# Kernel optimization log

Hardware: AMD Instinct MI355X
Metric: run time of the kernel (lower is better)

The kernel has to match this reference:

```python
import jax, jax.numpy as jnp
import numpy as np

# Static problem sizes (uniform ragged batch -> dense-packable)
B, NC, NP, C = 16, 128, 256, 128
HID = 2 * C            # mlp_hidden_scale * embedding_channels
COORD_SCALE = 5.0      # args.coord_scale
DIS_THRES = 10.0       # args.dis_map_thres
N_PROT = 16384         # total protein_whole residues
MAXN = 2 + NC + NP     # per-sample complex length (glb_c + compound + glb_p + pocket)


def setup_inputs() -> dict:
    key = jax.random.key(0)
    ks = jax.random.split(key, 12)
    protein_feats = jax.random.normal(ks[0], (N_PROT, 1280), jnp.float32)
    compound_feats = jax.random.normal(ks[1], (B * NC, 56), jnp.float32)
    complex_coords = jax.random.normal(ks[2], (B * MAXN, 3), jnp.float32) * 10.0
    dis_map = jax.random.uniform(ks[3], (B * NP * NC,), jnp.float32) * DIS_THRES
    keep_idx = jnp.sort(jax.random.randint(ks[4], (B * NP,), 0, N_PROT))
    glb_c = jnp.ones((1, C), jnp.float32)
    glb_p = jnp.ones((1, C), jnp.float32)
    # xavier_uniform with gain=0.001 ~ tiny weights
    W_prot = jax.random.normal(ks[5], (1280, C), jnp.float32) * 0.001
    b_prot = jnp.zeros((C,), jnp.float32)
    W_comp = jax.random.normal(ks[6], (56, C), jnp.float32) * 0.001
    b_comp = jnp.zeros((C,), jnp.float32)
    W1 = jax.random.normal(ks[7], (C, HID), jnp.float32) / np.sqrt(C)
    b1 = jnp.zeros((HID,), jnp.float32)
    W2 = jax.random.normal(ks[8], (HID, 1), jnp.float32) / np.sqrt(HID)
    b2 = jnp.zeros((1,), jnp.float32)
    return dict(protein_feats=protein_feats, compound_feats=compound_feats,
                complex_coords=complex_coords, dis_map=dis_map, keep_idx=keep_idx,
                glb_c=glb_c, glb_p=glb_p, W_prot=W_prot, b_prot=b_prot,
                W_comp=W_comp, b_comp=b_comp, W1=W1, b1=b1, W2=W2, b2=b2)


def reference(protein_feats, compound_feats, complex_coords, dis_map, keep_idx,
              glb_c, glb_p, W_prot, b_prot, W_comp, b_comp, W1, b1, W2, b2):
    # --- input projections + keepNode gather (pocket residues from whole protein)
    pocket_emb = (protein_feats[keep_idx] @ W_prot + b_prot).reshape(B, NP, C)
    compound_emb = (compound_feats @ W_comp + b_comp).reshape(B, NC, C)

    # --- ragged batch assembly: per-sample [glb_c, compound_i, glb_p, pocket_i]
    # (uniform sizes -> single dense concat replaces the Python loop of mask+cat)
    gc = jnp.broadcast_to(glb_c[None], (B, 1, C))
    gp = jnp.broadcast_to(glb_p[None], (B, 1, C))
    new_samples = jnp.concatenate([gc, compound_emb, gp, pocket_emb], axis=1)  # [B, MAXN, C]

    # --- stand-in pair embedding for EfficientMCAttModel output:
    # pair_embed_batched[b, i, j] over (glb_p+pocket) x (glb_c+compound)
    p_side = new_samples[:, NC + 1:, :]     # [B, NP+1, C]
    c_side = new_samples[:, :NC + 1, :]     # [B, NC+1, C]
    pair = p_side[:, :, None, :] + c_side[:, None, :, :]  # [B, NP+1, NC+1, C]

    # --- coordinates (normalize, split by segment/is_global layout)
    coords = (complex_coords / COORD_SCALE).reshape(B, MAXN, 3)
    compound_coords_n = coords[:, 1:NC + 1, :]   # [B, NC, 3]
    pocket_coords_n = coords[:, NC + 2:, :]      # [B, NP, 3]

    # --- cdist(pocket, compound)  [B, NP, NC]
    diff = pocket_coords_n[:, :, None, :] - compound_coords_n[:, None, :, :]
    dmap = jnp.sqrt(jnp.sum(diff * diff, axis=-1) + 1e-12)

    # --- distmap MLP on z = pair[:, 1:, 1:] then sigmoid * thres
    z = pair[:, 1:, 1:, :]                        # [B, NP, NC, C]
    h = jax.nn.relu(z @ W1 + b1)                  # [B, NP, NC, HID]
    logits = (h @ W2 + b2)[..., 0]                # [B, NP, NC]
    # z_mask = outer(pocket_mask, compound_mask) is all-True for uniform sizes
    y_pred = jax.nn.sigmoid(logits).reshape(-1) * DIS_THRES
    y_pred_by_coords = jnp.clip(dmap.reshape(-1) * COORD_SCALE, 0.0, DIS_THRES)

    compound_coords_out = compound_coords_n.reshape(-1, 3) * COORD_SCALE
    pocket_coords_out = pocket_coords_n.reshape(-1, 3) * COORD_SCALE
    compound_batch = jnp.repeat(jnp.arange(B, dtype=jnp.int32), NC)
    pocket_batch = jnp.repeat(jnp.arange(B, dtype=jnp.int32), NP)
    keepNode_less_5 = jnp.zeros((), jnp.int32)
    return (compound_coords_out, compound_batch, pocket_coords_out, pocket_batch,
            y_pred, y_pred_by_coords, dis_map, keepNode_less_5)
```

## Files before the change

kernel.cpp:

```cpp
#include <hip/hip_runtime.h>
#include <hip/hip_bf16.h>
#include <cstddef>


typedef __attribute__((ext_vector_type(8))) short short8v;
typedef __attribute__((ext_vector_type(4))) float f32x4;
typedef _Float16 half2v __attribute__((ext_vector_type(2)));
typedef _Float16 half8v __attribute__((ext_vector_type(8)));

__device__ __forceinline__ unsigned int f2bf(float x) {
    unsigned int u = __float_as_uint(x);
    return (u + 0x7fffu + ((u >> 16) & 1u)) >> 16;
}

__device__ __forceinline__ float dot8h(half8v r, half8v w, float acc) {
#if __has_builtin(__builtin_amdgcn_fdot2)
#pragma unroll
    for (int q = 0; q < 4; ++q) {
        half2v rq = {r[2 * q], r[2 * q + 1]};
        half2v wq = {w[2 * q], w[2 * q + 1]};
        acc = __builtin_amdgcn_fdot2(rq, wq, acc, false);
    }
#else
#pragma unroll
    for (int q = 0; q < 8; ++q) acc += (float)r[q] * (float)w[q];
#endif
    return acc;
}

#define WS_WTP   0u
#define WS_WTC   655360u
#define WS_BP1   688128u
#define WS_BC1   689152u
#define WS_W2H   690176u
#define WS_P1H   691200u
#define WS_PPH   3836928u

__global__ __launch_bounds__(256) void k_fusew(const float* __restrict__ Wp,
                                               const float* __restrict__ Wc,
                                               const float* __restrict__ bp,
                                               const float* __restrict__ bc,
                                               const float* __restrict__ W1,
                                               const float* __restrict__ b1,
                                               const float* __restrict__ W2,
                                               const float* __restrict__ coords,
                                               const float* __restrict__ dism,
                                               float* __restrict__ out,
                                               char* __restrict__ ws) {
    const int tid = threadIdx.x, bid = blockIdx.x;

    if (bid >= 168) {
        const int g = (bid - 168) * 256 + tid;
        {
            const float4* src = reinterpret_cast<const float4*>(dism + (size_t)g * 8);
            float4* dst = reinterpret_cast<float4*>(out + 1073152 + (size_t)g * 8);
            dst[0] = src[0]; dst[1] = src[1];
        }
        if (g < 6144) {
            const int row = g / 3, d = g - row * 3;
            const int bb2 = row >> 7, c = row & 127;
            const float x = coords[(size_t)(bb2 * 386 + 1 + c) * 3 + d];
            out[g] = (x / 5.0f) * 5.0f;
        }
        if (g < 2048) out[6144 + g] = (float)(g >> 7);
        if (g < 12288) {
            const int row = g / 3, d = g - row * 3;
            const int bb2 = row >> 8, p = row & 255;
            const float x = coords[(size_t)(bb2 * 386 + 130 + p) * 3 + d];
            out[8192 + g] = (x / 5.0f) * 5.0f;
        }
        if (g < 4096) out[20480 + g] = (float)(g >> 8);
        if (g == 0) out[1597440] = 0.0f;
        return;
    }

    __shared__ float Al[8][128];
    const int row0 = bid * 8;
    {
        const int r = tid >> 5, k4 = (tid & 31) * 4;
        const int rg = row0 + r;
        float4 v = make_float4(0.f, 0.f, 0.f, 0.f);
        if (rg < 1280)       v = *reinterpret_cast<const float4*>(Wp + (size_t)rg * 128 + k4);
        else if (rg < 1336)  v = *reinterpret_cast<const float4*>(Wc + (size_t)(rg - 1280) * 128 + k4);
        else if (rg == 1336) v = *reinterpret_cast<const float4*>(bp + k4);
        else if (rg == 1337) v = *reinterpret_cast<const float4*>(bc + k4);
        *reinterpret_cast<float4*>(&Al[r][k4]) = v;
    }
    __syncthreads();
    float acc[8];
#pragma unroll
    for (int r = 0; r < 8; ++r) acc[r] = 0.f;
#pragma unroll 4
    for (int k4 = 0; k4 < 128; k4 += 4) {
        float w0 = W1[(k4 + 0) * 256 + tid];
        float w1 = W1[(k4 + 1) * 256 + tid];
        float w2 = W1[(k4 + 2) * 256 + tid];
        float w3 = W1[(k4 + 3) * 256 + tid];
#pragma unroll
        for (int r = 0; r < 8; ++r) {
            float4 a = *reinterpret_cast<const float4*>(&Al[r][k4]);
            acc[r] += a.x * w0 + a.y * w1 + a.z * w2 + a.w * w3;
        }
    }
    if (bid < 160) {
        unsigned int w[4];
#pragma unroll
        for (int q = 0; q < 4; ++q)
            w[q] = f2bf(acc[2 * q]) | (f2bf(acc[2 * q + 1]) << 16);
        unsigned short* WtP = (unsigned short*)(ws + WS_WTP);
        *reinterpret_cast<uint4*>(WtP + (size_t)tid * 1280 + row0) = make_uint4(w[0], w[1], w[2], w[3]);
    } else if (bid < 167) {
        unsigned int w[4];
#pragma unroll
        for (int q = 0; q < 4; ++q)
            w[q] = f2bf(acc[2 * q]) | (f2bf(acc[2 * q + 1]) << 16);
        unsigned short* WtC = (unsigned short*)(ws + WS_WTC);
        *reinterpret_cast<uint4*>(WtC + (size_t)tid * 64 + (row0 - 1280)) = make_uint4(w[0], w[1], w[2], w[3]);
    } else {
        ((float*)(ws + WS_BP1))[tid] = acc[0] + b1[tid];
        ((float*)(ws + WS_BC1))[tid] = acc[1];
        ((_Float16*)(ws + WS_W2H))[tid] = (_Float16)W2[tid];
        unsigned short* WtC = (unsigned short*)(ws + WS_WTC);
        *reinterpret_cast<uint4*>(WtC + (size_t)tid * 64 + 56) = make_uint4(0, 0, 0, 0);
    }
}

struct AB { float4 ra[2]; uint4 rb[8]; };

__device__ __forceinline__ void load_tile(AB& t, bool pocket, int koff,
                                          const float* __restrict__ prot,
                                          const float* __restrict__ comp,
                                          const int* keepL, int m0,
                                          const unsigned short* __restrict__ Bt,
                                          int bstride, int tid) {
#pragma unroll
    for (int u = 0; u < 2; ++u) {
        const int unit = tid + 256 * u;
        const int r = unit >> 4, kc = unit & 15;
        float4 v = make_float4(0.f, 0.f, 0.f, 0.f);
        if (pocket) {
            v = *reinterpret_cast<const float4*>(prot + (size_t)keepL[r] * 1280 + koff + kc * 4);
        } else if (kc < 14) {
            v = *reinterpret_cast<const float4*>(comp + (size_t)(m0 + r - 4096) * 56 + kc * 4);
        }
        t.ra[u] = v;
    }
#pragma unroll
    for (int u = 0; u < 8; ++u) {
        const int unit = tid + 256 * u;
        const int col = unit >> 3, k8 = unit & 7;
        t.rb[u] = *reinterpret_cast<const uint4*>(Bt + (size_t)col * bstride + koff + k8 * 8);
    }
}

__device__ __forceinline__ void store_tile(const AB& t, char* As, char* Bs, int tid) {
#pragma unroll
    for (int u = 0; u < 2; ++u) {
        const int unit = tid + 256 * u;
        const int r = unit >> 4, kc = unit & 15;
        const float4 v = t.ra[u];
        const unsigned int lo = f2bf(v.x) | (f2bf(v.y) << 16);
        const unsigned int hi = f2bf(v.z) | (f2bf(v.w) << 16);
        const int wb = (r * 128 + kc * 8) ^ ((r & 7) << 4);
        *reinterpret_cast<uint2*>(As + wb) = make_uint2(lo, hi);
    }
#pragma unroll
    for (int u = 0; u < 8; ++u) {
        const int unit = tid + 256 * u;
        const int col = unit >> 3, k8 = unit & 7;
        const int wb = (col * 128 + k8 * 16) ^ ((col & 7) << 4);
        *reinterpret_cast<uint4*>(Bs + wb) = t.rb[u];
    }
}

__global__ __launch_bounds__(256) void k_gemm(const float* __restrict__ prot,
                                              const int* __restrict__ keep,
                                              const float* __restrict__ comp,
                                              char* __restrict__ ws) {
    __shared__ __align__(16) char As[32 * 64 * 2];
    __shared__ __align__(16) char Bs[256 * 64 * 2];
    __shared__ int keepL[32];
    const int tid = threadIdx.x;
    const int l = tid & 63, wn = tid >> 6;
    const int l15 = l & 15, lg = l >> 4;
    const int bid = blockIdx.x;
    const bool pocket = (bid < 512);
    const int ks = pocket ? (bid & 3) : 0;
    const int m0 = pocket ? ((bid >> 2) * 32) : (4096 + (bid - 512) * 32);
    const int koff0 = ks * 320;
    const int iters = pocket ? 5 : 1;
    const unsigned short* Bt = (const unsigned short*)(ws + (pocket ? WS_WTP : WS_WTC));
    const int bstride = pocket ? 1280 : 64;

    if (pocket && tid < 32) keepL[tid] = keep[m0 + tid];
    __syncthreads();

    f32x4 acc[2][4];
#pragma unroll
    for (int m = 0; m < 2; ++m)
#pragma unroll
        for (int n = 0; n < 4; ++n) acc[m][n] = (f32x4){0.f, 0.f, 0.f, 0.f};

    AB cur, nxt;
    load_tile(cur, pocket, koff0, prot, comp, keepL, m0, Bt, bstride, tid);

    for (int it = 0; it < iters; ++it) {
        if (it) __syncthreads();
        store_tile(cur, As, Bs, tid);
        __syncthreads();
        if (it + 1 < iters)
            load_tile(nxt, pocket, koff0 + (it + 1) * 64, prot, comp, keepL, m0, Bt, bstride, tid);
#pragma unroll
        for (int kstep = 0; kstep < 2; ++kstep) {
            const int kbyte = kstep * 64 + lg * 16;
            short8v a[2], b[4];
#pragma unroll
            for (int m = 0; m < 2; ++m) {
                const int row = m * 16 + l15;
                a[m] = *reinterpret_cast<const short8v*>(As + ((row * 128 + kbyte) ^ ((row & 7) << 4)));
            }
#pragma unroll
            for (int n = 0; n < 4; ++n) {
                const int col = wn * 64 + n * 16 + l15;
                b[n] = *reinterpret_cast<const short8v*>(Bs + ((col * 128 + kbyte) ^ ((col & 7) << 4)));
            }
#pragma unroll
            for (int m = 0; m < 2; ++m)
#pragma unroll
                for (int n = 0; n < 4; ++n)
                    acc[m][n] = __builtin_amdgcn_mfma_f32_16x16x32_bf16(a[m], b[n], acc[m][n], 0, 0, 0);
        }
        if (it + 1 < iters) cur = nxt;
    }

    if (pocket) {
        _Float16* dst = (_Float16*)(ws + WS_PPH + (size_t)ks * 2097152u);
        const float* bias = (const float*)(ws + WS_BP1);
#pragma unroll
        for (int m = 0; m < 2; ++m)
#pragma unroll
            for (int n = 0; n < 4; ++n) {
                const int col = wn * 64 + n * 16 + l15;
                const float bb = (ks == 0) ? bias[col] : 0.f;
#pragma unroll
                for (int i = 0; i < 4; ++i) {
                    const int row = m0 + m * 16 + lg * 4 + i;
                    dst[((size_t)row << 8) + col] = (_Float16)(acc[m][n][i] + bb);
                }
            }
    } else {
        const float* bias = (const float*)(ws + WS_BC1);
        _Float16* P1h = (_Float16*)(ws + WS_P1H);
#pragma unroll
        for (int m = 0; m < 2; ++m)
#pragma unroll
            for (int n = 0; n < 4; ++n) {
                const int col = wn * 64 + n * 16 + l15;
                const float bb = bias[col];
#pragma unroll
                for (int i = 0; i < 4; ++i) {
                    const int row = m0 + m * 16 + lg * 4 + i;
                    P1h[(size_t)row * 256 + col] = (_Float16)(acc[m][n][i] + bb);
                }
            }
    }
}

__global__ __launch_bounds__(256) void k_pair(const char* __restrict__ ws,
                                              const float* __restrict__ b2,
                                              const float* __restrict__ coords,
                                              float* __restrict__ out) {
    __shared__ __align__(16) char Ph[32 * 512];
    __shared__ __align__(16) char Ch[32 * 512];
    __shared__ __align__(16) _Float16 W2l[256];
    __shared__ float pcs[32][3], ccs[32][3];
    const int tid = threadIdx.x;
    const int b = blockIdx.z, p0 = blockIdx.y * 32, c0 = blockIdx.x * 32;
    const _Float16* P1h = (const _Float16*)(ws + WS_P1H);
    const _Float16* pp = (const _Float16*)(ws + WS_PPH);

#pragma unroll
    for (int u = 0; u < 4; ++u) {
        const int unit = tid + 256 * u;
        const int row = unit >> 5, h8 = unit & 31;
        const size_t base = (((size_t)(b * 256 + p0 + row)) << 8) + h8 * 8;
        const half8v s0 = *reinterpret_cast<const half8v*>(pp + base);
        const half8v s1 = *reinterpret_cast<const half8v*>(pp + 1048576u + base);
        const half8v s2 = *reinterpret_cast<const half8v*>(pp + 2097152u + base);
        const half8v s3 = *reinterpret_cast<const half8v*>(pp + 3145728u + base);
        const half8v t = (s0 + s1) + (s2 + s3);
        const int key = ((row ^ (row >> 2)) & 7) << 4;
        *reinterpret_cast<half8v*>(Ph + ((row * 512 + h8 * 16) ^ key)) = t;
    }
#pragma unroll
    for (int u = 0; u < 4; ++u) {
        const int unit = tid + 256 * u;
        const int row = unit >> 5, h8 = unit & 31;
        const uint4 v = *reinterpret_cast<const uint4*>(P1h + (size_t)(4096 + b * 128 + c0 + row) * 256 + h8 * 8);
        const int key = ((row ^ (row >> 2)) & 7) << 4;
        *reinterpret_cast<uint4*>(Ch + ((row * 512 + h8 * 16) ^ key)) = v;
    }
    if (tid < 32) {
        *reinterpret_cast<uint4*>(W2l + tid * 8) =
            *reinterpret_cast<const uint4*>((const _Float16*)(ws + WS_W2H) + tid * 8);
        const float* s = coords + (size_t)(b * 386 + 130 + p0 + tid) * 3;
        pcs[tid][0] = s[0] / 5.0f; pcs[tid][1] = s[1] / 5.0f; pcs[tid][2] = s[2] / 5.0f;
    } else if (tid < 64) {
        const int t = tid - 32;
        const float* s = coords + (size_t)(b * 386 + 1 + c0 + t) * 3;
        ccs[t][0] = s[0] / 5.0f; ccs[t][1] = s[1] / 5.0f; ccs[t][2] = s[2] / 5.0f;
    }
    __syncthreads();

    const int pi = tid >> 4, ci = tid & 15;
    float acc[2][2] = {{0.f, 0.f}, {0.f, 0.f}};
#pragma unroll 4
    for (int h8 = 0; h8 < 32; ++h8) {
        const half8v wv = *reinterpret_cast<const half8v*>((const char*)W2l + h8 * 16);
        half8v pf[2], cf[2];
#pragma unroll
        for (int i = 0; i < 2; ++i) {
            const int row = pi * 2 + i;
            const int key = ((row ^ (row >> 2)) & 7) << 4;
            pf[i] = *reinterpret_cast<const half8v*>(Ph + ((row * 512 + h8 * 16) ^ key));
        }
#pragma unroll
        for (int j = 0; j < 2; ++j) {
            const int row = ci * 2 + j;
            const int key = ((row ^ (row >> 2)) & 7) << 4;
            cf[j] = *reinterpret_cast<const half8v*>(Ch + ((row * 512 + h8 * 16) ^ key));
        }
#pragma unroll
        for (int i = 0; i < 2; ++i)
#pragma unroll
            for (int j = 0; j < 2; ++j) {
                half8v s = pf[i] + cf[j];
                half8v r = __builtin_elementwise_max(s, (half8v)0);
                acc[i][j] = dot8h(r, wv, acc[i][j]);
            }
    }

    const float bb = b2[0];
#pragma unroll
    for (int i = 0; i < 2; ++i) {
        const int pr = pi * 2 + i;
        float2 y2, yc2;
        float* yp = &y2.x; float* yq = &yc2.x;
#pragma unroll
        for (int j = 0; j < 2; ++j) {
            const int cr = ci * 2 + j;
            const float logit = acc[i][j] + bb;
            yp[j] = 10.0f / (1.0f + expf(-logit));
            const float dx = pcs[pr][0] - ccs[cr][0];
            const float dy = pcs[pr][1] - ccs[cr][1];
            const float dz = pcs[pr][2] - ccs[cr][2];
            const float d = sqrtf(dx * dx + dy * dy + dz * dz + 1e-12f);
            yq[j] = fminf(fmaxf(d * 5.0f, 0.0f), 10.0f);
        }
        const size_t o = (size_t)(b * 256 + p0 + pr) * 128 + c0 + ci * 2;
        *reinterpret_cast<float2*>(out + 24576 + o) = y2;
        *reinterpret_cast<float2*>(out + 548864 + o) = yc2;
    }
}

extern "C" void kernel_launch(void* const* d_in, const int* in_sizes, int n_in,
                              void* d_out, int out_size, void* d_ws, size_t ws_size,
                              hipStream_t stream) {
    const float* prot   = (const float*)d_in[0];
    const float* comp   = (const float*)d_in[1];
    const float* coords = (const float*)d_in[2];
    const float* dism   = (const float*)d_in[3];
    const int*   keep   = (const int*)d_in[4];
    const float* Wp = (const float*)d_in[7];
    const float* bp = (const float*)d_in[8];
    const float* Wc = (const float*)d_in[9];
    const float* bc = (const float*)d_in[10];
    const float* W1 = (const float*)d_in[11];
    const float* b1 = (const float*)d_in[12];
    const float* W2 = (const float*)d_in[13];
    const float* b2 = (const float*)d_in[14];
    float* out = (float*)d_out;
    char* ws = (char*)d_ws;

    k_fusew<<<424, 256, 0, stream>>>(Wp, Wc, bp, bc, W1, b1, W2, coords, dism, out, ws);
    k_gemm<<<576, 256, 0, stream>>>(prot, keep, comp, ws);
    k_pair<<<dim3(4, 8, 16), 256, 0, stream>>>(ws, b2, coords, out);
}
```

Baseline: 43.83 us.

## Split fused-weight and projection GEMM blocks across output-column halves

Both the weight-fusion kernel and the projection GEMM now split their 256-column output into two 128-column halves, each handled by a separate block, which doubles the grid sizes. The GEMM also reorders its block index so that the two halves and the k-split slices of the same row tile are scheduled close together. The goal is more parallelism and smaller per-block register and LDS footprint on a GPU with many CUs. In exchange, the A tile (gathered protein rows converted to bf16) is loaded and converted twice, once per half.

```diff
diff --git a/kernel.cpp b/kernel.cpp
--- a/kernel.cpp
+++ b/kernel.cpp
@@ -49,8 +49,8 @@
                                                char* __restrict__ ws) {
     const int tid = threadIdx.x, bid = blockIdx.x;
 
-    if (bid >= 168) {
-        const int g = (bid - 168) * 256 + tid;
+    if (bid >= 336) {
+        const int g = (bid - 336) * 256 + tid;
         {
             const float4* src = reinterpret_cast<const float4*>(dism + (size_t)g * 8);
             float4* dst = reinterpret_cast<float4*>(out + 1073152 + (size_t)g * 8);
@@ -75,7 +75,8 @@
     }
 
     __shared__ float Al[8][128];
-    const int row0 = bid * 8;
+    const int wb = bid >> 1, nh = bid & 1;
+    const int row0 = wb * 8;
     {
         const int r = tid >> 5, k4 = (tid & 31) * 4;
         const int rg = row0 + r;
@@ -87,47 +88,47 @@
         *reinterpret_cast<float4*>(&Al[r][k4]) = v;
     }
     __syncthreads();
-    float acc[8];
-#pragma unroll
-    for (int r = 0; r < 8; ++r) acc[r] = 0.f;
+    const int col = (tid & 127) + nh * 128;
+    const int rh = tid >> 7;
+    float acc[4] = {0.f, 0.f, 0.f, 0.f};
 #pragma unroll 4
     for (int k4 = 0; k4 < 128; k4 += 4) {
-        float w0 = W1[(k4 + 0) * 256 + tid];
-        float w1 = W1[(k4 + 1) * 256 + tid];
-        float w2 = W1[(k4 + 2) * 256 + tid];
-        float w3 = W1[(k4 + 3) * 256 + tid];
-#pragma unroll
-        for (int r = 0; r < 8; ++r) {
-            float4 a = *reinterpret_cast<const float4*>(&Al[r][k4]);
+        float w0 = W1[(k4 + 0) * 256 + col];
+        float w1 = W1[(k4 + 1) * 256 + col];
+        float w2 = W1[(k4 + 2) * 256 + col];
+        float w3 = W1[(k4 + 3) * 256 + col];
+#pragma unroll
+        for (int r = 0; r < 4; ++r) {
+            float4 a = *reinterpret_cast<const float4*>(&Al[rh * 4 + r][k4]);
             acc[r] += a.x * w0 + a.y * w1 + a.z * w2 + a.w * w3;
         }
     }
-    if (bid < 160) {
-        unsigned int w[4];
-#pragma unroll
-        for (int q = 0; q < 4; ++q)
-            w[q] = f2bf(acc[2 * q]) | (f2bf(acc[2 * q + 1]) << 16);
+    if (wb < 160) {
+        const unsigned int w0 = f2bf(acc[0]) | (f2bf(acc[1]) << 16);
+        const unsigned int w1 = f2bf(acc[2]) | (f2bf(acc[3]) << 16);
         unsigned short* WtP = (unsigned short*)(ws + WS_WTP);
-        *reinterpret_cast<uint4*>(WtP + (size_t)tid * 1280 + row0) = make_uint4(w[0], w[1], w[2], w[3]);
-    } else if (bid < 167) {
-        unsigned int w[4];
-#pragma unroll
-        for (int q = 0; q < 4; ++q)
-            w[q] = f2bf(acc[2 * q]) | (f2bf(acc[2 * q + 1]) << 16);
+        *reinterpret_cast<uint2*>(WtP + (size_t)col * 1280 + row0 + rh * 4) = make_uint2(w0, w1);
+    } else if (wb < 167) {
+        const unsigned int w0 = f2bf(acc[0]) | (f2bf(acc[1]) << 16);
+        const unsigned int w1 = f2bf(acc[2]) | (f2bf(acc[3]) << 16);
         unsigned short* WtC = (unsigned short*)(ws + WS_WTC);
-        *reinterpret_cast<uint4*>(WtC + (size_t)tid * 64 + (row0 - 1280)) = make_uint4(w[0], w[1], w[2], w[3]);
+        *reinterpret_cast<uint2*>(WtC + (size_t)col * 64 + (row0 - 1280) + rh * 4) = make_uint2(w0, w1);
     } else {
-        ((float*)(ws + WS_BP1))[tid] = acc[0] + b1[tid];
-        ((float*)(ws + WS_BC1))[tid] = acc[1];
-        ((_Float16*)(ws + WS_W2H))[tid] = (_Float16)W2[tid];
-        unsigned short* WtC = (unsigned short*)(ws + WS_WTC);
-        *reinterpret_cast<uint4*>(WtC + (size_t)tid * 64 + 56) = make_uint4(0, 0, 0, 0);
-    }
-}
-
-struct AB { float4 ra[2]; uint4 rb[8]; };
-
-__device__ __forceinline__ void load_tile(AB& t, bool pocket, int koff,
+        if (rh == 0) {
+            ((float*)(ws + WS_BP1))[col] = acc[0] + b1[col];
+            ((float*)(ws + WS_BC1))[col] = acc[1];
+        } else {
+            ((_Float16*)(ws + WS_W2H))[col] = (_Float16)W2[col];
+            unsigned short* WtC = (unsigned short*)(ws + WS_WTC);
+            *reinterpret_cast<uint2*>(WtC + (size_t)col * 64 + 56) = make_uint2(0, 0);
+            *reinterpret_cast<uint2*>(WtC + (size_t)col * 64 + 60) = make_uint2(0, 0);
+        }
+    }
+}
+
+struct AB { float4 ra[2]; uint4 rb[4]; };
+
+__device__ __forceinline__ void load_tile(AB& t, bool pocket, int koff, int nh,
                                           const float* __restrict__ prot,
                                           const float* __restrict__ comp,
                                           const int* keepL, int m0,
@@ -146,10 +147,10 @@
         t.ra[u] = v;
     }
 #pragma unroll
-    for (int u = 0; u < 8; ++u) {
+    for (int u = 0; u < 4; ++u) {
         const int unit = tid + 256 * u;
         const int col = unit >> 3, k8 = unit & 7;
-        t.rb[u] = *reinterpret_cast<const uint4*>(Bt + (size_t)col * bstride + koff + k8 * 8);
+        t.rb[u] = *reinterpret_cast<const uint4*>(Bt + (size_t)(nh * 128 + col) * bstride + koff + k8 * 8);
     }
 }
 
@@ -165,7 +166,7 @@
         *reinterpret_cast<uint2*>(As + wb) = make_uint2(lo, hi);
     }
 #pragma unroll
-    for (int u = 0; u < 8; ++u) {
+    for (int u = 0; u < 4; ++u) {
         const int unit = tid + 256 * u;
         const int col = unit >> 3, k8 = unit & 7;
         const int wb = (col * 128 + k8 * 16) ^ ((col & 7) << 4);
@@ -178,56 +179,67 @@
                                               const float* __restrict__ comp,
                                               char* __restrict__ ws) {
     __shared__ __align__(16) char As[32 * 64 * 2];
-    __shared__ __align__(16) char Bs[256 * 64 * 2];
+    __shared__ __align__(16) char Bs[128 * 64 * 2];
     __shared__ int keepL[32];
     const int tid = threadIdx.x;
     const int l = tid & 63, wn = tid >> 6;
     const int l15 = l & 15, lg = l >> 4;
     const int bid = blockIdx.x;
-    const bool pocket = (bid < 512);
-    const int ks = pocket ? (bid & 3) : 0;
-    const int m0 = pocket ? ((bid >> 2) * 32) : (4096 + (bid - 512) * 32);
-    const int koff0 = ks * 320;
-    const int iters = pocket ? 5 : 1;
-    const unsigned short* Bt = (const unsigned short*)(ws + (pocket ? WS_WTP : WS_WTC));
-    const int bstride = pocket ? 1280 : 64;
+    const bool pocket = (bid < 1024);
+    int m0, ks, nh, iters, koff0, bstride;
+    const unsigned short* Bt;
+    if (pocket) {
+        const int a = bid & 7, c = bid >> 4;
+        nh = (bid >> 3) & 1;
+        const int tile = a + (c << 3);
+        m0 = (tile >> 2) * 32;
+        ks = tile & 3;
+        koff0 = ks * 320; iters = 5;
+        Bt = (const unsigned short*)(ws + WS_WTP); bstride = 1280;
+    } else {
+        const int u = bid - 1024;
+        m0 = 4096 + (u >> 1) * 32;
+        nh = u & 1; ks = 0;
+        koff0 = 0; iters = 1;
+        Bt = (const unsigned short*)(ws + WS_WTC); bstride = 64;
+    }
 
     if (pocket && tid < 32) keepL[tid] = keep[m0 + tid];
     __syncthreads();
 
-    f32x4 acc[2][4];
+    f32x4 acc[2][2];
 #pragma unroll
     for (int m = 0; m < 2; ++m)
 #pragma unroll
-        for (int n = 0; n < 4; ++n) acc[m][n] = (f32x4){0.f, 0.f, 0.f, 0.f};
+        for (int n = 0; n < 2; ++n) acc[m][n] = (f32x4){0.f, 0.f, 0.f, 0.f};
 
     AB cur, nxt;
-    load_tile(cur, pocket, koff0, prot, comp, keepL, m0, Bt, bstride, tid);
+    load_tile(cur, pocket, koff0, nh, prot, comp, keepL, m0, Bt, bstride, tid);
 
     for (int it = 0; it < iters; ++it) {
         if (it) __syncthreads();
         store_tile(cur, As, Bs, tid);
         __syncthreads();
         if (it + 1 < iters)
-            load_tile(nxt, pocket, koff0 + (it + 1) * 64, prot, comp, keepL, m0, Bt, bstride, tid);
+            load_tile(nxt, pocket, koff0 + (it + 1) * 64, nh, prot, comp, keepL, m0, Bt, bstride, tid);
 #pragma unroll
         for (int kstep = 0; kstep < 2; ++kstep) {
             const int kbyte = kstep * 64 + lg * 16;
-            short8v a[2], b[4];
+            short8v a[2], b[2];
 #pragma unroll
             for (int m = 0; m < 2; ++m) {
                 const int row = m * 16 + l15;
                 a[m] = *reinterpret_cast<const short8v*>(As + ((row * 128 + kbyte) ^ ((row & 7) << 4)));
             }
 #pragma unroll
-            for (int n = 0; n < 4; ++n) {
-                const int col = wn * 64 + n * 16 + l15;
+            for (int n = 0; n < 2; ++n) {
+                const int col = wn * 32 + n * 16 + l15;
                 b[n] = *reinterpret_cast<const short8v*>(Bs + ((col * 128 + kbyte) ^ ((col & 7) << 4)));
             }
 #pragma unroll
             for (int m = 0; m < 2; ++m)
 #pragma unroll
-                for (int n = 0; n < 4; ++n)
+                for (int n = 0; n < 2; ++n)
                     acc[m][n] = __builtin_amdgcn_mfma_f32_16x16x32_bf16(a[m], b[n], acc[m][n], 0, 0, 0);
         }
         if (it + 1 < iters) cur = nxt;
@@ -239,8 +251,8 @@
 #pragma unroll
         for (int m = 0; m < 2; ++m)
 #pragma unroll
-            for (int n = 0; n < 4; ++n) {
-                const int col = wn * 64 + n * 16 + l15;
+            for (int n = 0; n < 2; ++n) {
+                const int col = nh * 128 + wn * 32 + n * 16 + l15;
                 const float bb = (ks == 0) ? bias[col] : 0.f;
 #pragma unroll
                 for (int i = 0; i < 4; ++i) {
@@ -254,8 +266,8 @@
 #pragma unroll
         for (int m = 0; m < 2; ++m)
 #pragma unroll
-            for (int n = 0; n < 4; ++n) {
-                const int col = wn * 64 + n * 16 + l15;
+            for (int n = 0; n < 2; ++n) {
+                const int col = nh * 128 + wn * 32 + n * 16 + l15;
                 const float bb = bias[col];
 #pragma unroll
                 for (int i = 0; i < 4; ++i) {
@@ -382,7 +394,7 @@
     float* out = (float*)d_out;
     char* ws = (char*)d_ws;
 
-    k_fusew<<<424, 256, 0, stream>>>(Wp, Wc, bp, bc, W1, b1, W2, coords, dism, out, ws);
-    k_gemm<<<576, 256, 0, stream>>>(prot, keep, comp, ws);
+    k_fusew<<<592, 256, 0, stream>>>(Wp, Wc, bp, bc, W1, b1, W2, coords, dism, out, ws);
+    k_gemm<<<1152, 256, 0, stream>>>(prot, keep, comp, ws);
     k_pair<<<dim3(4, 8, 16), 256, 0, stream>>>(ws, b2, coords, out);
 }
```

New measurement: 39.80 us. -9.2%, faster.
